# Optimization experiments

Measured on AMD Instinct MI355X. Metric: run time of the kernel, lower is better.

The kernel has to match this reference:

```python
import jax, jax.numpy as jnp
import numpy as np

DIM = 64
POS_H = 64
ATTN_H = 4 * DIM
B, N = 2, 512


def setup_inputs() -> dict:
    key = jax.random.key(0)
    ks = jax.random.split(key, 20)
    g = lambda k, shape, fan_in: jax.random.normal(k, shape, jnp.float32) / np.sqrt(fan_in)
    return {
        "x": jax.random.normal(ks[0], (B, N, DIM), jnp.float32),
        "pos": jax.random.normal(ks[1], (B, N, 3), jnp.float32),
        "prev_w": g(ks[2], (DIM, DIM), DIM), "prev_b": jnp.zeros((DIM,), jnp.float32),
        "q_w": g(ks[3], (DIM, DIM), DIM),
        "k_w": g(ks[4], (DIM, DIM), DIM),
        "v_w": g(ks[5], (DIM, DIM), DIM),
        "pos_w1": g(ks[6], (3, POS_H), 3), "pos_b1": jnp.zeros((POS_H,), jnp.float32),
        "pos_w2": g(ks[7], (POS_H, DIM), POS_H), "pos_b2": jnp.zeros((DIM,), jnp.float32),
        "attn_w1": g(ks[8], (DIM, ATTN_H), DIM), "attn_b1": jnp.zeros((ATTN_H,), jnp.float32),
        "attn_w2": g(ks[9], (ATTN_H, DIM), ATTN_H), "attn_b2": jnp.zeros((DIM,), jnp.float32),
        "fin_w": g(ks[10], (DIM, DIM), DIM), "fin_b": jnp.zeros((DIM,), jnp.float32),
    }


def reference(x, pos, prev_w, prev_b, q_w, k_w, v_w,
              pos_w1, pos_b1, pos_w2, pos_b2,
              attn_w1, attn_b1, attn_w2, attn_b2, fin_w, fin_b):
    # prev_linear
    x1 = x @ prev_w + prev_b                              # [B,N,D]
    q = x1 @ q_w                                          # [B,N,D]
    k = x1 @ k_w
    v = x1 @ v_w
    # relative position embedding: [B,i,j,3] -> MLP -> [B,i,j,D]
    rel_pos = pos[:, :, None, :] - pos[:, None, :, :]
    rpe = jax.nn.relu(rel_pos @ pos_w1 + pos_b1) @ pos_w2 + pos_b2
    # per-pair qk difference + attn MLP -> vector (channel-wise) attention logits
    qk_rel = q[:, :, None, :] - k[:, None, :, :]          # [B,i,j,D]
    sim = jax.nn.relu((qk_rel + rpe) @ attn_w1 + attn_b1) @ attn_w2 + attn_b2  # [B,i,j,D]
    # v indexed by j, plus pairwise positional embedding
    v2 = v[:, None, :, :] + rpe                           # [B,i,j,D]
    attn = jax.nn.softmax(sim, axis=2)                    # softmax over j (dim=-2 of [B,i,j,D])
    agg = jnp.einsum('bijd,bijd->bid', attn, v2)          # [B,N,D]
    x_out = agg @ fin_w + fin_b + x1                      # final_linear + residual
    return (x_out, pos)
```

## Files before the change

### kernel.cpp

```cpp
#include <hip/hip_runtime.h>

typedef __attribute__((ext_vector_type(4))) float f32x4;
typedef __attribute__((ext_vector_type(8))) __bf16 bf16x8;
typedef __attribute__((ext_vector_type(4))) __bf16 bf16x4;
typedef __attribute__((ext_vector_type(2))) unsigned int u32x2;

template<int OFF>
__device__ __forceinline__ u32x2 tr_read_o(unsigned base){
    u32x2 d;
    asm volatile("ds_read_b64_tr_b16 %0, %1 offset:%c2"
                 : "=v"(d) : "v"(base), "i"(OFF));
    return d;
}
__device__ __forceinline__ bf16x8 frag_cat(u32x2 a, u32x2 b){
    union { u32x2 u[2]; bf16x8 f; } c; c.u[0] = a; c.u[1] = b; return c.f;
}


__global__ void ptb_pre(const float* __restrict__ x,
                        const float* __restrict__ pos,
                        const float* __restrict__ prev_w,
                        const float* __restrict__ prev_b,
                        const float* __restrict__ q_w,
                        const float* __restrict__ k_w,
                        const float* __restrict__ v_w,
                        const float* __restrict__ pos_w2,
                        const float* __restrict__ attn_w1,
                        const float* __restrict__ attn_b1,
                        float* __restrict__ ws,
                        float* __restrict__ out)
{
    const int bid = blockIdx.x;
    const int tid = threadIdx.x;
    __shared__ float xr[256], x1r[256], qsh[256], ksh[256], vsh[256];

    float wcol[64];
    #pragma unroll
    for (int c = 0; c < 64; ++c) wcol[c] = attn_w1[c*256 + tid];

    if (bid >= 256){
        xr[tid] = pos_w2[(bid - 256)*256 + tid];
        __syncthreads();
        float* Wp = ws + 655360;
        #pragma unroll
        for (int r = 0; r < 4; ++r){
            float s = 0.f;
            #pragma unroll 16
            for (int c = 0; c < 64; ++c) s += xr[r*64 + c] * wcol[c];
            Wp[((bid - 256)*4 + r)*256 + tid] = s;
        }
        return;
    }

    const int rr  = tid >> 6, d = tid & 63;
    const int row = bid*4 + rr;
    xr[tid] = x[row*64 + d];
    __syncthreads();
    float a = prev_b[d];
    #pragma unroll 16
    for (int c = 0; c < 64; ++c) a += xr[rr*64 + c] * prev_w[c*64 + d];
    x1r[tid] = a;
    ws[row*64 + d] = a;
    __syncthreads();
    float qv = 0.f, kv = 0.f, vv = 0.f;
    #pragma unroll 16
    for (int c = 0; c < 64; ++c){
        float t = x1r[rr*64 + c];
        qv += t * q_w[c*64 + d];
        kv += t * k_w[c*64 + d];
        vv += t * v_w[c*64 + d];
    }
    qsh[tid] = qv; ksh[tid] = kv; vsh[tid] = vv;
    if (tid < 12) out[65536 + bid*12 + tid] = pos[bid*12 + tid];
    __syncthreads();

    ws[65536 + bid*256 + tid] = vsh[(tid & 3)*64 + (tid >> 2)];

    float* Q1  = ws + 131072;
    float* K1s = ws + 393216;
    const float bb = attn_b1[tid];
    float sq[4], sk[4];
    #pragma unroll
    for (int r = 0; r < 4; ++r){ sq[r] = bb; sk[r] = 0.f; }
    #pragma unroll 16
    for (int c = 0; c < 64; ++c){
        const float wv = wcol[c];
        #pragma unroll
        for (int r = 0; r < 4; ++r){
            sq[r] += qsh[r*64 + c] * wv;
            sk[r] += ksh[r*64 + c] * wv;
        }
    }
    #pragma unroll
    for (int r = 0; r < 4; ++r) Q1[(bid*4 + r)*256 + tid] = sq[r];
    f32x4 kvec = {sk[0], sk[1], sk[2], sk[3]};
    *(f32x4*)&K1s[bid*1024 + tid*4] = kvec;
}

__global__ __launch_bounds__(256) void ptb_main(
    const float* __restrict__ pos,
    const float* __restrict__ pos_w1, const float* __restrict__ pos_b1,
    const float* __restrict__ pos_w2, const float* __restrict__ pos_b2,
    const float* __restrict__ attn_w2, const float* __restrict__ attn_b2,
    const float* __restrict__ fin_w, const float* __restrict__ fin_b,
    const float* __restrict__ ws, float* __restrict__ out)
{
    const int blk = blockIdx.x;
    const int b   = blk >> 9;
    const int i   = blk & 511;
    const int tid = threadIdx.x;
    const int w   = tid >> 6;
    const int l   = tid & 63;
    const int lg  = l >> 4;
    const int ln  = l & 15;

    __shared__ __bf16 sH1[64][64];
    __shared__ __align__(16) char sHT[18432];
    __shared__ float sPW1[192], sPB1[64], sAGG[64], sPOSI[3];

    const float* x1p = ws;
    const float* vs  = ws + 65536;
    const float* Q1  = ws + 131072;
    const float* K1s = ws + 393216;
    const float* Wp  = ws + 655360;

    if (tid < 64) sPB1[tid] = pos_b1[tid];
    if (tid >= 64 && tid < 256) sPW1[tid - 64] = pos_w1[tid - 64];
    if (tid < 3) sPOSI[tid] = pos[(b*512 + i)*3 + tid];

    const int dch  = w*16 + ln;
    const int Ew   = w*64;
    const int swzA = (ln & 7) << 3;

    const float LOG2E = 1.44269504088896f;

    bf16x8 w1f[2][4];
    #pragma unroll
    for (int kf = 0; kf < 2; ++kf)
        #pragma unroll
        for (int et = 0; et < 4; ++et)
            #pragma unroll
            for (int ii = 0; ii < 8; ++ii)
                w1f[kf][et][ii] = (__bf16)Wp[(kf*32 + lg*8 + ii)*256 + Ew + et*16 + ln];
    bf16x8 w2f[8];
    #pragma unroll
    for (int kf = 0; kf < 8; ++kf)
        #pragma unroll
        for (int ii = 0; ii < 8; ++ii)
            w2f[kf][ii] = (__bf16)(attn_w2[(kf*32 + lg*8 + ii)*64 + dch] * LOG2E);
    bf16x8 pwfw[2];
    #pragma unroll
    for (int kf = 0; kf < 2; ++kf)
        #pragma unroll
        for (int ii = 0; ii < 8; ++ii)
            pwfw[kf][ii] = (__bf16)pos_w2[(kf*32 + lg*8 + ii)*64 + dch];

    float Q1b[4];
    #pragma unroll
    for (int et = 0; et < 4; ++et) Q1b[et] = Q1[blk*256 + Ew + et*16 + ln];
    const float pb2v = pos_b2[dch];
    const float b2v  = attn_b2[dch] * LOG2E;

    const unsigned sHTb = (unsigned)(unsigned long long)&sHT[0];
    const unsigned trbase = sHTb + (unsigned)(lg*288 + ln*8);

    float mrun = -1e30f, srun = 0.f, arun = 0.f;

    bf16x8 h1r0, h1r1;
    auto computeA = [&](int j0a){
        const float* pj = &pos[(b*512 + j0a + w*16 + ln)*3];
        const float r0 = sPOSI[0] - pj[0];
        const float r1 = sPOSI[1] - pj[1];
        const float r2 = sPOSI[2] - pj[2];
        bf16x8 o[2];
        #pragma unroll
        for (int kf = 0; kf < 2; ++kf){
            const int hb = kf*32 + lg*8;
            f32x4 wa0 = *(const f32x4*)&sPW1[      hb],   wa1 = *(const f32x4*)&sPW1[      hb+4];
            f32x4 wb0 = *(const f32x4*)&sPW1[ 64 + hb],   wb1 = *(const f32x4*)&sPW1[ 64 + hb+4];
            f32x4 wc0 = *(const f32x4*)&sPW1[128 + hb],   wc1 = *(const f32x4*)&sPW1[128 + hb+4];
            f32x4 bb0 = *(const f32x4*)&sPB1[      hb],   bb1 = *(const f32x4*)&sPB1[      hb+4];
            #pragma unroll
            for (int ii = 0; ii < 4; ++ii){
                float hv0 = bb0[ii] + r0*wa0[ii] + r1*wb0[ii] + r2*wc0[ii];
                float hv1 = bb1[ii] + r0*wa1[ii] + r1*wb1[ii] + r2*wc1[ii];
                o[kf][ii]   = (__bf16)fmaxf(hv0, 0.f);
                o[kf][ii+4] = (__bf16)fmaxf(hv1, 0.f);
            }
        }
        h1r0 = o[0]; h1r1 = o[1];
    };
    auto commitA = [&](){
        *(bf16x8*)&sH1[w*16 + ln][(     lg*8) ^ swzA] = h1r0;
        *(bf16x8*)&sH1[w*16 + ln][(32 + lg*8) ^ swzA] = h1r1;
    };

    __syncthreads();
    computeA(0);
    commitA();

    #pragma unroll 1
    for (int t = 0; t < 8; ++t){
        const int j0 = t << 6;
        __syncthreads();
        if (t < 7) computeA(j0 + 64);
        #pragma unroll 1
        for (int hb = 0; hb < 2; ++hb){
            f32x4 rcs[2];
            #pragma unroll
            for (int jj = 0; jj < 2; ++jj){
                const int jrow = hb*32 + jj*16;
                const int krow = ((b*512 + j0 + jrow) >> 2) + lg;
                const bf16x8 af0 = *(const bf16x8*)&sH1[jrow + ln][(     lg*8) ^ swzA];
                const bf16x8 af1 = *(const bf16x8*)&sH1[jrow + ln][(32 + lg*8) ^ swzA];
                f32x4 accs[4];
                #pragma unroll
                for (int et = 0; et < 4; ++et){
                    const f32x4 kw4 = *(const f32x4*)&K1s[krow*1024 + (Ew + et*16 + ln)*4];
                    const f32x4 qv4 = {Q1b[et], Q1b[et], Q1b[et], Q1b[et]};
                    accs[et] = qv4 - kw4;
                }
                __builtin_amdgcn_s_setprio(1);
                #pragma unroll
                for (int et = 0; et < 4; ++et)
                    accs[et] = __builtin_amdgcn_mfma_f32_16x16x32_bf16(af0, w1f[0][et], accs[et], 0, 0, 0);
                #pragma unroll
                for (int et = 0; et < 4; ++et)
                    accs[et] = __builtin_amdgcn_mfma_f32_16x16x32_bf16(af1, w1f[1][et], accs[et], 0, 0, 0);
                f32x4 rcv = {pb2v, pb2v, pb2v, pb2v};
                rcv = __builtin_amdgcn_mfma_f32_16x16x32_bf16(af0, pwfw[0], rcv, 0, 0, 0);
                rcv = __builtin_amdgcn_mfma_f32_16x16x32_bf16(af1, pwfw[1], rcv, 0, 0, 0);
                rcs[jj] = rcv;
                __builtin_amdgcn_s_setprio(0);
                #pragma unroll
                for (int et = 0; et < 4; ++et){
                    bf16x4 hp;
                    #pragma unroll
                    for (int ri = 0; ri < 4; ++ri) hp[ri] = (__bf16)fmaxf(accs[et][ri], 0.f);
                    *(bf16x4*)(sHT + (jj*64 + w*16 + et*4 + (ln>>2))*144
                                   + (ln&3)*32 + lg*8) = hp;
                }
            }
            __syncthreads();
            if (hb == 1 && t < 7) commitA();
            f32x4 accv[2], vvv[2];
            #pragma unroll
            for (int jj = 0; jj < 2; ++jj){
                const int vrow = ((b*512 + j0 + hb*32 + jj*16) >> 2) + lg;
                vvv[jj] = *(const f32x4*)&vs[vrow*256 + dch*4];
            }
            u32x2 h0[16], h1[16];
            #define TR2A(KF) \
                h0[(KF)*2]   = tr_read_o<(KF)*1152      >(trbase); \
                h0[(KF)*2+1] = tr_read_o<(KF)*1152 + 144>(trbase);
            TR2A(0) TR2A(1) TR2A(2) TR2A(3) TR2A(4) TR2A(5) TR2A(6) TR2A(7)
            #undef TR2A
            asm volatile("s_waitcnt lgkmcnt(8)" ::: "memory");
            __builtin_amdgcn_sched_barrier(0);
            {
                f32x4 a0 = {b2v, b2v, b2v, b2v};
                f32x4 a1 = {0.f, 0.f, 0.f, 0.f};
                __builtin_amdgcn_s_setprio(1);
                a0 = __builtin_amdgcn_mfma_f32_16x16x32_bf16(frag_cat(h0[0], h0[1]), w2f[0], a0, 0, 0, 0);
                a1 = __builtin_amdgcn_mfma_f32_16x16x32_bf16(frag_cat(h0[2], h0[3]), w2f[1], a1, 0, 0, 0);
                a0 = __builtin_amdgcn_mfma_f32_16x16x32_bf16(frag_cat(h0[4], h0[5]), w2f[2], a0, 0, 0, 0);
                a1 = __builtin_amdgcn_mfma_f32_16x16x32_bf16(frag_cat(h0[6], h0[7]), w2f[3], a1, 0, 0, 0);
                __builtin_amdgcn_s_setprio(0);
                const unsigned trb1 = trbase + 9216u;
                #define TR2B(KF) \
                    h1[(KF)*2]   = tr_read_o<(KF)*1152      >(trb1); \
                    h1[(KF)*2+1] = tr_read_o<(KF)*1152 + 144>(trb1);
                TR2B(0) TR2B(1) TR2B(2) TR2B(3)
                asm volatile("s_waitcnt lgkmcnt(8)" ::: "memory");
                __builtin_amdgcn_sched_barrier(0);
                __builtin_amdgcn_s_setprio(1);
                a0 = __builtin_amdgcn_mfma_f32_16x16x32_bf16(frag_cat(h0[8],  h0[9]),  w2f[4], a0, 0, 0, 0);
                a1 = __builtin_amdgcn_mfma_f32_16x16x32_bf16(frag_cat(h0[10], h0[11]), w2f[5], a1, 0, 0, 0);
                a0 = __builtin_amdgcn_mfma_f32_16x16x32_bf16(frag_cat(h0[12], h0[13]), w2f[6], a0, 0, 0, 0);
                a1 = __builtin_amdgcn_mfma_f32_16x16x32_bf16(frag_cat(h0[14], h0[15]), w2f[7], a1, 0, 0, 0);
                __builtin_amdgcn_s_setprio(0);
                accv[0] = a0 + a1;
                TR2B(4) TR2B(5) TR2B(6) TR2B(7)
                #undef TR2B
            }
            asm volatile("s_waitcnt lgkmcnt(8)" ::: "memory");
            __builtin_amdgcn_sched_barrier(0);
            {
                f32x4 a0 = {b2v, b2v, b2v, b2v};
                f32x4 a1 = {0.f, 0.f, 0.f, 0.f};
                __builtin_amdgcn_s_setprio(1);
                a0 = __builtin_amdgcn_mfma_f32_16x16x32_bf16(frag_cat(h1[0], h1[1]), w2f[0], a0, 0, 0, 0);
                a1 = __builtin_amdgcn_mfma_f32_16x16x32_bf16(frag_cat(h1[2], h1[3]), w2f[1], a1, 0, 0, 0);
                a0 = __builtin_amdgcn_mfma_f32_16x16x32_bf16(frag_cat(h1[4], h1[5]), w2f[2], a0, 0, 0, 0);
                a1 = __builtin_amdgcn_mfma_f32_16x16x32_bf16(frag_cat(h1[6], h1[7]), w2f[3], a1, 0, 0, 0);
                __builtin_amdgcn_s_setprio(0);
                asm volatile("s_waitcnt lgkmcnt(0)" ::: "memory");
                __builtin_amdgcn_sched_barrier(0);
                __builtin_amdgcn_s_setprio(1);
                a0 = __builtin_amdgcn_mfma_f32_16x16x32_bf16(frag_cat(h1[8],  h1[9]),  w2f[4], a0, 0, 0, 0);
                a1 = __builtin_amdgcn_mfma_f32_16x16x32_bf16(frag_cat(h1[10], h1[11]), w2f[5], a1, 0, 0, 0);
                a0 = __builtin_amdgcn_mfma_f32_16x16x32_bf16(frag_cat(h1[12], h1[13]), w2f[6], a0, 0, 0, 0);
                a1 = __builtin_amdgcn_mfma_f32_16x16x32_bf16(frag_cat(h1[14], h1[15]), w2f[7], a1, 0, 0, 0);
                __builtin_amdgcn_s_setprio(0);
                accv[1] = a0 + a1;
            }
            float tmax = fmaxf(fmaxf(fmaxf(accv[0][0], accv[0][1]),
                                     fmaxf(accv[0][2], accv[0][3])),
                               fmaxf(fmaxf(accv[1][0], accv[1][1]),
                                     fmaxf(accv[1][2], accv[1][3])));
            tmax = fmaxf(tmax, __shfl_xor(tmax, 16));
            tmax = fmaxf(tmax, __shfl_xor(tmax, 32));
            const float mnew  = fmaxf(mrun, tmax);
            const float scale = __builtin_amdgcn_exp2f(mrun - mnew);
            srun *= scale; arun *= scale; mrun = mnew;
            #pragma unroll
            for (int jj = 0; jj < 2; ++jj)
                #pragma unroll
                for (int ri = 0; ri < 4; ++ri){
                    const float p = __builtin_amdgcn_exp2f(accv[jj][ri] - mnew);
                    srun += p;
                    arun += p * (vvv[jj][ri] + rcs[jj][ri]);
                }
            if (hb == 0) __syncthreads();
        }
    }

    arun += __shfl_xor(arun, 16); arun += __shfl_xor(arun, 32);
    srun += __shfl_xor(srun, 16); srun += __shfl_xor(srun, 32);
    if (lg == 0) sAGG[dch] = arun / srun;
    __syncthreads();

    if (tid < 64){
        float a = fin_b[tid] + x1p[blk*64 + tid];
        #pragma unroll 16
        for (int c = 0; c < 64; ++c) a += sAGG[c] * fin_w[c*64 + tid];
        out[blk*64 + tid] = a;
    }
}

extern "C" void kernel_launch(void* const* d_in, const int* in_sizes, int n_in,
                              void* d_out, int out_size, void* d_ws, size_t ws_size,
                              hipStream_t stream)
{
    const float* x       = (const float*)d_in[0];
    const float* pos     = (const float*)d_in[1];
    const float* prev_w  = (const float*)d_in[2];
    const float* prev_b  = (const float*)d_in[3];
    const float* q_w     = (const float*)d_in[4];
    const float* k_w     = (const float*)d_in[5];
    const float* v_w     = (const float*)d_in[6];
    const float* pos_w1  = (const float*)d_in[7];
    const float* pos_b1  = (const float*)d_in[8];
    const float* pos_w2  = (const float*)d_in[9];
    const float* pos_b2  = (const float*)d_in[10];
    const float* attn_w1 = (const float*)d_in[11];
    const float* attn_b1 = (const float*)d_in[12];
    const float* attn_w2 = (const float*)d_in[13];
    const float* attn_b2 = (const float*)d_in[14];
    const float* fin_w   = (const float*)d_in[15];
    const float* fin_b   = (const float*)d_in[16];
    float* out = (float*)d_out;
    float* ws  = (float*)d_ws;

    ptb_pre<<<272, 256, 0, stream>>>(x, pos, prev_w, prev_b, q_w, k_w, v_w,
                                     pos_w2, attn_w1, attn_b1, ws, out);
    ptb_main<<<1024, 256, 0, stream>>>(pos, pos_w1, pos_b1, pos_w2, pos_b2,
                                       attn_w2, attn_b2, fin_w, fin_b, ws, out);
}
```

Before: 107.1 us.

## Split key range across two blocks per query with split-softmax merge kernel

Each query row's 512 keys are now split across two blocks (2048 blocks instead of 1024). Each block writes its partial max, sum and weighted accumulator to workspace, and a new small kernel merges the partials and applies the final linear layer plus residual. The position-MLP prefetch is also restructured to keep only the three position deltas in registers across the loop, instead of the packed hidden activations. This is meant to improve load balance and GPU occupancy. In exchange it adds an extra kernel launch, a workspace round trip, and per-block weight-loading overhead that is now duplicated across twice as many blocks.

```diff
diff --git a/kernel.cpp b/kernel.cpp
--- a/kernel.cpp
+++ b/kernel.cpp
@@ -102,12 +102,13 @@
     const float* __restrict__ pos_w1, const float* __restrict__ pos_b1,
     const float* __restrict__ pos_w2, const float* __restrict__ pos_b2,
     const float* __restrict__ attn_w2, const float* __restrict__ attn_b2,
-    const float* __restrict__ fin_w, const float* __restrict__ fin_b,
-    const float* __restrict__ ws, float* __restrict__ out)
+    const float* __restrict__ ws, float* __restrict__ wsp)
 {
     const int blk = blockIdx.x;
-    const int b   = blk >> 9;
-    const int i   = blk & 511;
+    const int ib  = blk >> 1;
+    const int jh  = blk & 1;
+    const int b   = ib >> 9;
+    const int i   = ib & 511;
     const int tid = threadIdx.x;
     const int w   = tid >> 6;
     const int l   = tid & 63;
@@ -116,9 +117,8 @@
 
     __shared__ __bf16 sH1[64][64];
     __shared__ __align__(16) char sHT[18432];
-    __shared__ float sPW1[192], sPB1[64], sAGG[64], sPOSI[3];
-
-    const float* x1p = ws;
+    __shared__ float sPW1[192], sPB1[64], sPOSI[3];
+
     const float* vs  = ws + 65536;
     const float* Q1  = ws + 131072;
     const float* K1s = ws + 393216;
@@ -157,7 +157,7 @@
 
     float Q1b[4];
     #pragma unroll
-    for (int et = 0; et < 4; ++et) Q1b[et] = Q1[blk*256 + Ew + et*16 + ln];
+    for (int et = 0; et < 4; ++et) Q1b[et] = Q1[ib*256 + Ew + et*16 + ln];
     const float pb2v = pos_b2[dch];
     const float b2v  = attn_b2[dch] * LOG2E;
 
@@ -166,13 +166,7 @@
 
     float mrun = -1e30f, srun = 0.f, arun = 0.f;
 
-    bf16x8 h1r0, h1r1;
-    auto computeA = [&](int j0a){
-        const float* pj = &pos[(b*512 + j0a + w*16 + ln)*3];
-        const float r0 = sPOSI[0] - pj[0];
-        const float r1 = sPOSI[1] - pj[1];
-        const float r2 = sPOSI[2] - pj[2];
-        bf16x8 o[2];
+    auto stageA = [&](float r0, float r1, float r2){
         #pragma unroll
         for (int kf = 0; kf < 2; ++kf){
             const int hb = kf*32 + lg*8;
@@ -180,30 +174,38 @@
             f32x4 wb0 = *(const f32x4*)&sPW1[ 64 + hb],   wb1 = *(const f32x4*)&sPW1[ 64 + hb+4];
             f32x4 wc0 = *(const f32x4*)&sPW1[128 + hb],   wc1 = *(const f32x4*)&sPW1[128 + hb+4];
             f32x4 bb0 = *(const f32x4*)&sPB1[      hb],   bb1 = *(const f32x4*)&sPB1[      hb+4];
+            bf16x8 h1f;
             #pragma unroll
             for (int ii = 0; ii < 4; ++ii){
                 float hv0 = bb0[ii] + r0*wa0[ii] + r1*wb0[ii] + r2*wc0[ii];
                 float hv1 = bb1[ii] + r0*wa1[ii] + r1*wb1[ii] + r2*wc1[ii];
-                o[kf][ii]   = (__bf16)fmaxf(hv0, 0.f);
-                o[kf][ii+4] = (__bf16)fmaxf(hv1, 0.f);
-            }
+                h1f[ii]   = (__bf16)fmaxf(hv0, 0.f);
+                h1f[ii+4] = (__bf16)fmaxf(hv1, 0.f);
+            }
+            *(bf16x8*)&sH1[w*16 + ln][(kf*32 + lg*8) ^ swzA] = h1f;
         }
-        h1r0 = o[0]; h1r1 = o[1];
     };
-    auto commitA = [&](){
-        *(bf16x8*)&sH1[w*16 + ln][(     lg*8) ^ swzA] = h1r0;
-        *(bf16x8*)&sH1[w*16 + ln][(32 + lg*8) ^ swzA] = h1r1;
+    auto posdelta = [&](int j0a, float& r0, float& r1, float& r2){
+        const float* pj = &pos[(b*512 + j0a + w*16 + ln)*3];
+        r0 = sPOSI[0] - pj[0];
+        r1 = sPOSI[1] - pj[1];
+        r2 = sPOSI[2] - pj[2];
     };
 
-    __syncthreads();
-    computeA(0);
-    commitA();
+    const int t0 = jh*4;
+    __syncthreads();
+    {
+        float r0, r1, r2;
+        posdelta(t0 << 6, r0, r1, r2);
+        stageA(r0, r1, r2);
+    }
 
     #pragma unroll 1
-    for (int t = 0; t < 8; ++t){
+    for (int t = t0; t < t0 + 4; ++t){
         const int j0 = t << 6;
         __syncthreads();
-        if (t < 7) computeA(j0 + 64);
+        float pr0 = 0.f, pr1 = 0.f, pr2 = 0.f;
+        if (t < t0 + 3) posdelta(j0 + 64, pr0, pr1, pr2);
         #pragma unroll 1
         for (int hb = 0; hb < 2; ++hb){
             f32x4 rcs[2];
@@ -242,7 +244,7 @@
                 }
             }
             __syncthreads();
-            if (hb == 1 && t < 7) commitA();
+            if (hb == 1 && t < t0 + 3) stageA(pr0, pr1, pr2);
             f32x4 accv[2], vvv[2];
             #pragma unroll
             for (int jj = 0; jj < 2; ++jj){
@@ -327,15 +329,34 @@
 
     arun += __shfl_xor(arun, 16); arun += __shfl_xor(arun, 32);
     srun += __shfl_xor(srun, 16); srun += __shfl_xor(srun, 32);
-    if (lg == 0) sAGG[dch] = arun / srun;
-    __syncthreads();
-
-    if (tid < 64){
-        float a = fin_b[tid] + x1p[blk*64 + tid];
-        #pragma unroll 16
-        for (int c = 0; c < 64; ++c) a += sAGG[c] * fin_w[c*64 + tid];
-        out[blk*64 + tid] = a;
-    }
+    if (lg == 0){
+        float* P = wsp + 671744 + blk*192;
+        P[dch]       = mrun;
+        P[64 + dch]  = srun;
+        P[128 + dch] = arun;
+    }
+}
+
+__global__ void ptb_fin(const float* __restrict__ fin_w,
+                        const float* __restrict__ fin_b,
+                        const float* __restrict__ ws,
+                        float* __restrict__ out)
+{
+    const int ib  = blockIdx.x;
+    const int tid = threadIdx.x;
+    const float* P0 = ws + 671744 + (ib*2    )*192;
+    const float* P1 = ws + 671744 + (ib*2 + 1)*192;
+    __shared__ float sAGG[64];
+    const float m0 = P0[tid], s0 = P0[64+tid], a0 = P0[128+tid];
+    const float m1 = P1[tid], s1 = P1[64+tid], a1 = P1[128+tid];
+    const float M  = fmaxf(m0, m1);
+    const float e0 = exp2f(m0 - M), e1 = exp2f(m1 - M);
+    sAGG[tid] = (a0*e0 + a1*e1) / (s0*e0 + s1*e1);
+    __syncthreads();
+    float a = fin_b[tid] + ws[ib*64 + tid];
+    #pragma unroll 16
+    for (int c = 0; c < 64; ++c) a += sAGG[c] * fin_w[c*64 + tid];
+    out[ib*64 + tid] = a;
 }
 
 extern "C" void kernel_launch(void* const* d_in, const int* in_sizes, int n_in,
@@ -364,6 +385,7 @@
 
     ptb_pre<<<272, 256, 0, stream>>>(x, pos, prev_w, prev_b, q_w, k_w, v_w,
                                      pos_w2, attn_w1, attn_b1, ws, out);
-    ptb_main<<<1024, 256, 0, stream>>>(pos, pos_w1, pos_b1, pos_w2, pos_b2,
-                                       attn_w2, attn_b2, fin_w, fin_b, ws, out);
-}
+    ptb_main<<<2048, 256, 0, stream>>>(pos, pos_w1, pos_b1, pos_w2, pos_b2,
+                                       attn_w2, attn_b2, ws, ws);
+    ptb_fin<<<1024, 64, 0, stream>>>(fin_w, fin_b, ws, out);
+}
```

After: 109.7 us. 1.02x slower.
